# Performance work log

Measured on AMD Instinct MI355X. Metric: run time of the kernel, lower is better.

## Reference

```python
import jax, jax.numpy as jnp
import numpy as np

B, N, D = 32, 2048, 320

def _init(key, shape, fan_in):
    return jax.random.normal(key, shape, dtype=jnp.float32) / np.sqrt(fan_in).astype(np.float32)

def setup_inputs() -> dict:
    key = jax.random.key(0)
    ks = jax.random.split(key, 11)
    return {
        "x": jax.random.normal(ks[0], (B, N, D), dtype=jnp.float32),
        # downs MLP: 320->160->80
        "W1": _init(ks[1], (320, 160), 320), "b1": jnp.zeros((160,), jnp.float32),
        "W2": _init(ks[2], (160, 80), 160),  "b2": jnp.zeros((80,), jnp.float32),
        # GraphConv1d layers: 80->40, 40->5
        "Wg1": _init(ks[3], (80, 40), 80),   "bg1": jnp.zeros((40,), jnp.float32),
        "Wg2": _init(ks[4], (40, 5), 40),    "bg2": jnp.zeros((5,), jnp.float32),
        # final classifier: 5->2
        "Wf": _init(ks[5], (5, 2), 5),       "bf": jnp.zeros((2,), jnp.float32),
    }

def _euclidean_adj(h):
    # h: [B, N, C] -> row-softmax of negative squared pairwise Euclidean distance [B, N, N]
    sq = jnp.sum(h * h, axis=-1, keepdims=True)               # [B, N, 1]
    d2 = sq - 2.0 * jnp.einsum('bnc,bmc->bnm', h, h) + jnp.swapaxes(sq, -1, -2)
    return jax.nn.softmax(-d2, axis=-1)

def _graph_conv(h, W, b):
    a = _euclidean_adj(h)                                     # dynamic adjacency
    agg = jnp.einsum('bnm,bmc->bnc', a, h)                    # neighbor aggregation
    return jax.nn.relu(agg @ W + b)

def reference(x, W1, b1, W2, b2, Wg1, bg1, Wg2, bg2, Wf, bf):
    h = jax.nn.relu(x @ W1 + b1)          # [B, N, 160]
    h = jax.nn.relu(h @ W2 + b2)          # [B, N, 80]
    h = _graph_conv(h, Wg1, bg1)          # [B, N, 40]
    h = _graph_conv(h, Wg2, bg2)          # [B, N, 5]
    h = jnp.mean(h, axis=1)               # Mean() over nodes -> [B, 5]
    logits = h @ Wf + bf                  # [B, 2]
    return jax.nn.softmax(logits, axis=-1)
```

## Files before the change

kernel.cpp:

```cpp
#include <hip/hip_runtime.h>
#include <math.h>

#define BB 32
#define NN 2048
#define D_IN 320
#define H1 160
#define H2 80
#define H4 5

typedef __attribute__((ext_vector_type(8))) short short8;
typedef __attribute__((ext_vector_type(4))) short short4v;
typedef __attribute__((ext_vector_type(4))) float f32x4;
typedef __attribute__((ext_vector_type(16))) float f32x16;

__device__ inline ushort f2bf(float f) {
    union { float f; unsigned u; } v; v.f = f;
    unsigned r = v.u + 0x7fff + ((v.u >> 16) & 1);
    return (ushort)(r >> 16);
}
__device__ inline float bf2f(ushort u) {
    union { float f; unsigned u; } v; v.u = ((unsigned)u) << 16;
    return v.f;
}
__device__ inline unsigned pkbf(float hi, float lo) {
    union { float f; unsigned u; } a, b; a.f = hi; b.f = lo;
    return __builtin_amdgcn_perm(a.u + 0x8000u, b.u + 0x8000u, 0x07060302u);
}
__device__ inline float fexp2(float x) {
    float r;
    asm("v_exp_f32 %0, %1" : "=v"(r) : "v"(x));
    return r;
}
union U2S { unsigned u[2]; short4v s; };
union U4S { unsigned u[4]; short8 s; short4v h[2]; };

#define LOG2E  1.44269504088896340736f
#define TWOL2E 2.88539008177792681472f

__global__ __launch_bounds__(256) void prep_weights_kernel(
    const float* __restrict__ W1, const float* __restrict__ W2,
    const float* __restrict__ Wg1, const float* __restrict__ bg1,
    const float* __restrict__ Wg2, const float* __restrict__ bg2,
    ushort* __restrict__ Wt1, ushort* __restrict__ Wt2,
    ushort* __restrict__ Wg1B, float* __restrict__ bg1P,
    ushort* __restrict__ Wg2A, float* __restrict__ bg2P)
{
    const int id0 = blockIdx.x * 256 + threadIdx.x;
    const int stride = gridDim.x * 256;
    for (int i = id0; i < H1 * D_IN; i += stride) {
        const int j = i / D_IN, c = i % D_IN;
        Wt1[i] = f2bf(W1[c * H1 + j]);
    }
    for (int i = id0; i < H2 * H1; i += stride) {
        const int j = i / H1, c = i % H1;
        Wt2[i] = f2bf(W2[c * H2 + j]);
    }
    for (int i = id0; i < 48 * 96; i += stride) {
        const int j = i / 96, c = i % 96;
        Wg1B[i] = (j < 40 && c < 80) ? f2bf(Wg1[c * 40 + j]) : (ushort)0;
    }
    for (int i = id0; i < 32 * 48; i += stride) {
        const int j = i / 48, c = i % 48;
        const int c4 = c & 15;
        const int pos = (c & ~15) + (c4 & 3) + (((c4 >> 3) & 1) << 2) + (((c4 >> 2) & 1) << 3);
        Wg2A[j * 48 + pos] = (j < 5 && c < 40) ? f2bf(Wg2[c * 5 + j]) : (ushort)0;
    }
    if (id0 < 64) bg1P[id0] = (id0 < 40) ? bg1[id0] : 0.f;
    if (id0 < 32) bg2P[id0] = (id0 < 5) ? bg2[id0] : 0.f;
}

__global__ __launch_bounds__(256) void mlp_mfma_kernel(
    const float* __restrict__ x,
    const ushort* __restrict__ Wt1, const float* __restrict__ b1,
    const ushort* __restrict__ Wt2, const float* __restrict__ b2,
    const ushort* __restrict__ Wg1B,
    ushort* __restrict__ h2, ushort* __restrict__ V1T, float* __restrict__ sq2)
{
    constexpr int XST  = 72;
    constexpr int W1ST = 72;
    constexpr int H1ST = 168;
    constexpr int RST  = 104;

    __shared__ __attribute__((aligned(16))) ushort h1t[64 * H1ST];
    __shared__ __attribute__((aligned(16))) ushort ws1[H1 * W1ST];
    __shared__ float b1s[H1];
    __shared__ float b2s[H2];

    ushort* xs = h1t;

    const int t = threadIdx.x;
    const int lane = t & 63, w = t >> 6;
    const int colid = lane & 15, quad = lane >> 4;
    const int i = blockIdx.x;
    const int b = ((i & 7) << 2) + ((i >> 3) & 3);
    const int n0 = (i >> 5) * 64;
    const int row0 = b * NN + n0;

    if (t < H1) b1s[t] = b1[t];
    if (t < H2) b2s[t] = b2[t];

    f32x4 c1[10];
    #pragma unroll
    for (int ns = 0; ns < 10; ++ns) c1[ns] = (f32x4){0.f, 0.f, 0.f, 0.f};

    float4 xr[4];
    short8 wr[5];
    {
        #pragma unroll
        for (int i2 = 0; i2 < 4; ++i2) {
            const int id = t + i2 * 256, row = id >> 4, c4 = id & 15;
            xr[i2] = *(const float4*)&x[(size_t)(row0 + row) * D_IN + c4 * 4];
        }
        #pragma unroll
        for (int i2 = 0; i2 < 5; ++i2) {
            const int id = t + i2 * 256, j = id >> 3, part = id & 7;
            wr[i2] = *(const short8*)&Wt1[j * D_IN + part * 8];
        }
    }

    for (int kc = 0; kc < 5; ++kc) {
        if (kc) __syncthreads();
        #pragma unroll
        for (int i2 = 0; i2 < 4; ++i2) {
            const int id = t + i2 * 256, row = id >> 4, c4 = id & 15;
            uint2 up;
            up.x = pkbf(xr[i2].y, xr[i2].x);
            up.y = pkbf(xr[i2].w, xr[i2].z);
            *(uint2*)&xs[row * XST + c4 * 4] = up;
        }
        #pragma unroll
        for (int i2 = 0; i2 < 5; ++i2) {
            const int id = t + i2 * 256, j = id >> 3, part = id & 7;
            *(short8*)&ws1[j * W1ST + part * 8] = wr[i2];
        }
        __syncthreads();
        if (kc < 4) {
            const int k0 = (kc + 1) * 64;
            #pragma unroll
            for (int i2 = 0; i2 < 4; ++i2) {
                const int id = t + i2 * 256, row = id >> 4, c4 = id & 15;
                xr[i2] = *(const float4*)&x[(size_t)(row0 + row) * D_IN + k0 + c4 * 4];
            }
            #pragma unroll
            for (int i2 = 0; i2 < 5; ++i2) {
                const int id = t + i2 * 256, j = id >> 3, part = id & 7;
                wr[i2] = *(const short8*)&Wt1[j * D_IN + k0 + part * 8];
            }
        }

        short8 af[2];
        #pragma unroll
        for (int kf = 0; kf < 2; ++kf)
            af[kf] = *(const short8*)&xs[(w * 16 + colid) * XST + kf * 32 + quad * 8];
        #pragma unroll
        for (int ns = 0; ns < 10; ++ns) {
            #pragma unroll
            for (int kf = 0; kf < 2; ++kf) {
                const short8 bf = *(const short8*)&ws1[(ns * 16 + colid) * W1ST + kf * 32 + quad * 8];
                c1[ns] = __builtin_amdgcn_mfma_f32_16x16x32_bf16(af[kf], bf, c1[ns], 0, 0, 0);
            }
        }
    }
    __syncthreads();

    #pragma unroll
    for (int ns = 0; ns < 10; ++ns) {
        const float bj = b1s[ns * 16 + colid];
        #pragma unroll
        for (int r = 0; r < 4; ++r)
            h1t[(w * 16 + quad * 4 + r) * H1ST + ns * 16 + colid] =
                f2bf(fmaxf(c1[ns][r] + bj, 0.f));
    }
    __asm__ volatile("s_waitcnt lgkmcnt(0)" ::: "memory");

    short8 a2[5];
    #pragma unroll
    for (int kf = 0; kf < 5; ++kf)
        a2[kf] = *(const short8*)&h1t[(w * 16 + colid) * H1ST + kf * 32 + quad * 8];

    f32x4 c2[5];
    #pragma unroll
    for (int js = 0; js < 5; ++js) {
        f32x4 acc = (f32x4){0.f, 0.f, 0.f, 0.f};
        #pragma unroll
        for (int kf = 0; kf < 5; ++kf) {
            const short8 wb = *(const short8*)&Wt2[(js * 16 + colid) * H1 + kf * 32 + quad * 8];
            acc = __builtin_amdgcn_mfma_f32_16x16x32_bf16(a2[kf], wb, acc, 0, 0, 0);
        }
        c2[js] = acc;
    }
    __syncthreads();

    ushort* h2row = h1t;
    float rsq[4] = {0.f, 0.f, 0.f, 0.f};
    #pragma unroll
    for (int js = 0; js < 5; ++js) {
        const float bj = b2s[js * 16 + colid];
        #pragma unroll
        for (int r = 0; r < 4; ++r) {
            const ushort u = f2bf(fmaxf(c2[js][r] + bj, 0.f));
            const float vv = bf2f(u);
            rsq[r] += vv * vv;
            h2[(size_t)(row0 + w * 16 + quad * 4 + r) * 80 + js * 16 + colid] = u;
            h2row[(w * 16 + quad * 4 + r) * RST + js * 16 + colid] = u;
        }
    }
    {
        const int zr = t >> 2, zc = t & 3;
        *(short4v*)&h2row[zr * RST + 80 + zc * 4] = (short4v){0, 0, 0, 0};
    }
    __asm__ volatile("s_waitcnt lgkmcnt(0)" ::: "memory");

    short8 a3[3];
    #pragma unroll
    for (int kf = 0; kf < 3; ++kf)
        a3[kf] = *(const short8*)&h2row[(w * 16 + colid) * RST + kf * 32 + quad * 8];

    f32x4 c3[3];
    #pragma unroll
    for (int js = 0; js < 3; ++js) {
        f32x4 acc = (f32x4){0.f, 0.f, 0.f, 0.f};
        #pragma unroll
        for (int kf = 0; kf < 3; ++kf) {
            const short8 wb = *(const short8*)&Wg1B[(js * 16 + colid) * 96 + kf * 32 + quad * 8];
            acc = __builtin_amdgcn_mfma_f32_16x16x32_bf16(a3[kf], wb, acc, 0, 0, 0);
        }
        c3[js] = acc;
    }

    #pragma unroll
    for (int m = 1; m <= 8; m <<= 1)
        #pragma unroll
        for (int r = 0; r < 4; ++r) rsq[r] += __shfl_xor(rsq[r], m);
    if (colid == 0) {
        #pragma unroll
        for (int r = 0; r < 4; ++r)
            sq2[(size_t)row0 + w * 16 + quad * 4 + r] = rsq[r] * 0.5f;
    }

    ushort* Tbuf = ws1;
    #pragma unroll
    for (int js = 0; js < 3; ++js)
        #pragma unroll
        for (int r = 0; r < 4; ++r)
            Tbuf[(js * 16 + colid) * 72 + w * 16 + quad * 4 + r] = f2bf(c3[js][r]);
    __syncthreads();
    const short8 ones8 = {16256, 16256, 16256, 16256, 16256, 16256, 16256, 16256};
    for (int id = t; id < 48 * 8; id += 256) {
        const int row = id >> 3, part = id & 7;
        const short8 val = (row == 40) ? ones8 : *(const short8*)&Tbuf[row * 72 + part * 8];
        *(short8*)&V1T[((size_t)b * 48 + row) * NN + n0 + part * 8] = val;
    }
}

template<int CK, int CV, int CVS, int ONES_CH, bool HAS_OUT, bool DO_MEAN, int C_OUT>
__global__ __launch_bounds__(256, 2) void attn_conv_kernel(
    const ushort* __restrict__ h, const ushort* __restrict__ hT,
    const float* __restrict__ sqg,
    const ushort* __restrict__ WtP, const float* __restrict__ biasP,
    ushort* __restrict__ ho, ushort* __restrict__ hoT, float* __restrict__ sqo,
    float* __restrict__ mean_out)
{
    constexpr int CF   = CK / 16;
    constexpr int CSV  = CV / 32;
    constexpr int KST  = CK + 8;
    constexpr int VST  = 64 + 8;
    constexpr int KPR  = CK / 8;
    constexpr int KTOT = 64 * KPR;
    constexpr int NK   = (KTOT + 255) / 256;
    constexpr int VTOT = CVS * 8;
    constexpr int NV   = (VTOT + 255) / 256;
    constexpr int TST  = 136;
    constexpr int CS1  = ONES_CH / 32;
    constexpr int R1   = ((ONES_CH % 32) / 8) * 4 + (ONES_CH & 3);
    constexpr int BUFN = 64 * KST + CVS * VST;
    constexpr int NIT  = NN / 64;
    constexpr int NRND = NIT / 2;

    __shared__ __attribute__((aligned(16))) ushort ldsbuf[4][BUFN];
    __shared__ __attribute__((aligned(16))) float sqs[4][64];

    const int t = threadIdx.x;
    const int lane = t & 63, w = t >> 6;
    const int m32 = lane & 31, hl = lane >> 5;
    const int i = blockIdx.x;
    const int b = ((i & 7) << 2) + ((i >> 3) & 3);
    const int n0blk = (i >> 5) * 128;
    const int qrow = n0blk + w * 32 + m32;

    short8 qf[CF];
    {
        const ushort* qr = h + ((size_t)b * NN + qrow) * CK;
        #pragma unroll
        for (int c = 0; c < CF; ++c)
            qf[c] = *(const short8*)&qr[c * 16 + hl * 8];
    }
    const float nsqn = -sqg[(size_t)b * NN + qrow];

    f32x16 o[CSV];
    #pragma unroll
    for (int cs = 0; cs < CSV; ++cs)
        #pragma unroll
        for (int r = 0; r < 16; ++r) o[cs][r] = 0.f;

    short8 kregA[NK], vregA[NV]; float sqregA = 0.f;
    short8 kregB[NK], vregB[NV]; float sqregB = 0.f;

    auto loadTile = [&](int n1, short8 (&kreg)[NK], short8 (&vreg)[NV], float& sqreg) {
        const ushort* hsrc = h + ((size_t)b * NN + n1) * CK;
        #pragma unroll
        for (int i2 = 0; i2 < NK; ++i2) {
            const int id = t + i2 * 256;
            if (KTOT % 256 == 0 || id < KTOT)
                kreg[i2] = *(const short8*)&hsrc[id * 8];
        }
        #pragma unroll
        for (int i2 = 0; i2 < NV; ++i2) {
            const int id = t + i2 * 256;
            if (VTOT % 256 == 0 || id < VTOT) {
                const int c = id >> 3, pt = id & 7;
                vreg[i2] = *(const short8*)&hT[((size_t)b * CVS + c) * NN + n1 + pt * 8];
            }
        }
        if (t < 64) sqreg = sqg[(size_t)b * NN + n1 + t];
    };
    auto stageTile = [&](int buf, const short8 (&kreg)[NK], const short8 (&vreg)[NV], float sqreg) {
        ushort* Kd = ldsbuf[buf];
        ushort* Vd = ldsbuf[buf] + 64 * KST;
        #pragma unroll
        for (int i2 = 0; i2 < NK; ++i2) {
            const int id = t + i2 * 256;
            if (KTOT % 256 == 0 || id < KTOT) {
                const int row = id / KPR, pt = id % KPR;
                *(short8*)&Kd[row * KST + pt * 8] = kreg[i2];
            }
        }
        #pragma unroll
        for (int i2 = 0; i2 < NV; ++i2) {
            const int id = t + i2 * 256;
            if (VTOT % 256 == 0 || id < VTOT) {
                const int c = id >> 3, pt = id & 7;
                const int colb = ((pt >> 1) << 4) + ((pt & 1) << 2);
                U4S vv; vv.s = vreg[i2];
                *(short4v*)&Vd[c * VST + colb]     = vv.h[0];
                *(short4v*)&Vd[c * VST + colb + 8] = vv.h[1];
            }
        }
        if (t < 64) sqs[buf][t] = sqreg;
    };

    auto preloadK = [&](const ushort* Krow, short8 (&kf)[2][CF]) {
        #pragma unroll
        for (int T = 0; T < 2; ++T)
            #pragma unroll
            for (int c = 0; c < CF; ++c)
                kf[T][c] = *(const short8*)&Krow[(T * 32 + m32) * KST + c * 16 + hl * 8];
    };
    auto initST = [&](int buf, f32x16& s0, f32x16& s1) {
        #pragma unroll
        for (int g = 0; g < 4; ++g) {
            const f32x4 sm0 = *(const f32x4*)&sqs[buf][g * 8 + hl * 4];
            const f32x4 sm1 = *(const f32x4*)&sqs[buf][32 + g * 8 + hl * 4];
            #pragma unroll
            for (int r2 = 0; r2 < 4; ++r2) {
                s0[g * 4 + r2] = nsqn - sm0[r2];
                s1[g * 4 + r2] = nsqn - sm1[r2];
            }
        }
    };
    auto smfma = [&](short8 (&kf)[2][CF], f32x16& s0, f32x16& s1) {
        #pragma unroll
        for (int c = 0; c < CF; ++c) {
            s0 = __builtin_amdgcn_mfma_f32_32x32x16_bf16(kf[0][c], qf[c], s0, 0, 0, 0);
            s1 = __builtin_amdgcn_mfma_f32_32x32x16_bf16(kf[1][c], qf[c], s1, 0, 0, 0);
        }
    };
    auto readV = [&](const ushort* Vcol, short8 (&vf)[2][2][CSV]) {
        const short8 z8 = {0, 0, 0, 0, 0, 0, 0, 0};
        #pragma unroll
        for (int T = 0; T < 2; ++T)
            #pragma unroll
            for (int c = 0; c < 2; ++c)
                #pragma unroll
                for (int cs = 0; cs < CSV; ++cs) {
                    const int row = cs * 32 + m32;
                    vf[T][c][cs] = (row < CVS)
                        ? *(const short8*)&Vcol[row * VST + (T * 2 + c) * 16 + hl * 8]
                        : z8;
                }
    };
    auto expPV = [&](const f32x16& s0, const f32x16& s1, const short8 (&vf)[2][2][CSV]) {
        #pragma unroll
        for (int T = 0; T < 2; ++T) {
            const f32x16& st = T ? s1 : s0;
            float p[16];
            #pragma unroll
            for (int g = 0; g < 4; ++g)
                #pragma unroll
                for (int r2 = 0; r2 < 4; ++r2)
                    p[g * 4 + r2] = fexp2(st[g * 4 + r2] * TWOL2E);
            #pragma unroll
            for (int c = 0; c < 2; ++c) {
                U4S pk_;
                #pragma unroll
                for (int bq = 0; bq < 4; ++bq)
                    pk_.u[bq] = pkbf(p[c * 8 + bq * 2 + 1], p[c * 8 + bq * 2]);
                #pragma unroll
                for (int cs = 0; cs < CSV; ++cs)
                    o[cs] = __builtin_amdgcn_mfma_f32_32x32x16_bf16(vf[T][c][cs], pk_.s, o[cs], 0, 0, 0);
            }
        }
    };

    loadTile(0, kregA, vregA, sqregA);
    loadTile(64, kregB, vregB, sqregB);
    stageTile(0, kregA, vregA, sqregA);
    stageTile(1, kregB, vregB, sqregB);
    __syncthreads();
    loadTile(128, kregA, vregA, sqregA);
    loadTile(192, kregB, vregB, sqregB);

    #pragma unroll 1
    for (int k = 0; k < NRND; ++k) {
        const int p = k & 1;
        const ushort* K0 = ldsbuf[2 * p];
        const ushort* K1 = ldsbuf[2 * p + 1];

        f32x16 s00, s01, s10, s11;
        short8 kf[2][CF];
        preloadK(K0, kf);
        initST(2 * p, s00, s01);
        initST(2 * p + 1, s10, s11);

        if (k < NRND - 1) {
            stageTile(2 * (1 - p), kregA, vregA, sqregA);
            stageTile(2 * (1 - p) + 1, kregB, vregB, sqregB);
        }
        if (k < NRND - 2) {
            loadTile((2 * k + 4) * 64, kregA, vregA, sqregA);
            loadTile((2 * k + 5) * 64, kregB, vregB, sqregB);
        }

        smfma(kf, s00, s01);
        preloadK(K1, kf);
        smfma(kf, s10, s11);

        short8 vf[2][2][CSV];
        readV(K0 + 64 * KST, vf);
        expPV(s00, s01, vf);
        readV(K1 + 64 * KST, vf);
        expPV(s10, s11, vf);

        if (k < NRND - 1) __syncthreads();
    }

    float rsv = (hl == 0) ? o[CS1][R1] : 0.f;
    rsv += __shfl_xor(rsv, 32);
    const float rinv = 1.f / rsv;

    if constexpr (DO_MEAN) {
        float msum[4];
        #pragma unroll
        for (int r2 = 0; r2 < 4; ++r2)
            msum[r2] = fmaxf(o[0][r2] * rinv + biasP[hl * 4 + r2], 0.f);
        #pragma unroll
        for (int s = 1; s <= 16; s <<= 1)
            #pragma unroll
            for (int r2 = 0; r2 < 4; ++r2) msum[r2] += __shfl_xor(msum[r2], s);
        if (m32 == 0) {
            if (hl == 0) {
                #pragma unroll
                for (int r2 = 0; r2 < 4; ++r2)
                    atomicAdd(&mean_out[b * C_OUT + r2], msum[r2] * (1.f / NN));
            } else {
                atomicAdd(&mean_out[b * C_OUT + 4], msum[0] * (1.f / NN));
            }
        }
    }

    if constexpr (HAS_OUT) {
        float vv[CSV][16];
        float rsq = 0.f;
        #pragma unroll
        for (int cs = 0; cs < CSV; ++cs) {
            #pragma unroll
            for (int g = 0; g < 4; ++g) {
                const int jb = cs * 32 + g * 8 + hl * 4;
                const f32x4 bv = *(const f32x4*)&biasP[jb];
                float v[4];
                #pragma unroll
                for (int r2 = 0; r2 < 4; ++r2) {
                    float val = fmaxf(o[cs][g * 4 + r2] * rinv + bv[r2], 0.f);
                    if (cs == CS1 && g * 4 + r2 == R1) val = 0.f;
                    v[r2] = val;
                    vv[cs][g * 4 + r2] = val;
                }
                if (jb < 48) {
                    U2S uo;
                    uo.u[0] = pkbf(v[1], v[0]);
                    uo.u[1] = pkbf(v[3], v[2]);
                    *(short4v*)&ho[((size_t)b * NN + qrow) * 48 + jb] = uo.s;
                    #pragma unroll
                    for (int r2 = 0; r2 < 4; ++r2) {
                        const float vs = bf2f((ushort)(uo.u[r2 >> 1] >> ((r2 & 1) * 16)));
                        rsq += vs * vs;
                    }
                }
            }
        }
        const float rsq2 = rsq + __shfl_xor(rsq, 32);
        if (hl == 0) sqo[(size_t)b * NN + qrow] = rsq2 * 0.5f;

        short8 ob2[3];
        #pragma unroll
        for (int cc = 0; cc < 3; ++cc) {
            const int cs = cc >> 1, c2 = cc & 1;
            U4S ob_;
            #pragma unroll
            for (int bq = 0; bq < 4; ++bq)
                ob_.u[bq] = pkbf(vv[cs][c2 * 8 + bq * 2 + 1], vv[cs][c2 * 8 + bq * 2]);
            ob2[cc] = ob_.s;
        }
        f32x16 acc;
        #pragma unroll
        for (int r = 0; r < 16; ++r) acc[r] = 0.f;
        #pragma unroll
        for (int cc = 0; cc < 3; ++cc) {
            const short8 wa = *(const short8*)&WtP[(size_t)m32 * 48 + cc * 16 + hl * 8];
            acc = __builtin_amdgcn_mfma_f32_32x32x16_bf16(wa, ob2[cc], acc, 0, 0, 0);
        }

        ushort* Tbuf = (ushort*)ldsbuf;
        #pragma unroll
        for (int g = 0; g < 2; ++g)
            #pragma unroll
            for (int r2 = 0; r2 < 4; ++r2)
                Tbuf[(g * 8 + hl * 4 + r2) * TST + w * 32 + m32] = f2bf(acc[g * 4 + r2]);
        __syncthreads();
        const short8 ones8 = {16256, 16256, 16256, 16256, 16256, 16256, 16256, 16256};
        {
            const int row = t >> 4, part = t & 15;
            const short8 val = (row == 8) ? ones8
                             : *(const short8*)&Tbuf[row * TST + part * 8];
            *(short8*)&hoT[((size_t)b * 16 + row) * NN + n0blk + part * 8] = val;
        }
    }
}

__global__ __launch_bounds__(64) void final_kernel(
    const float* __restrict__ mean, const float* __restrict__ Wf,
    const float* __restrict__ bf, float* __restrict__ out)
{
    const int t = threadIdx.x;
    const int b = t >> 1, k = t & 1;
    float acc = bf[k];
    #pragma unroll
    for (int c = 0; c < H4; ++c) acc += mean[b * H4 + c] * Wf[c * 2 + k];
    const float other = __shfl_xor(acc, 1);
    const float mx = fmaxf(acc, other);
    const float e  = __expf(acc - mx);
    const float eo = __expf(other - mx);
    out[t] = e / (e + eo);
}

extern "C" void kernel_launch(void* const* d_in, const int* in_sizes, int n_in,
                              void* d_out, int out_size, void* d_ws, size_t ws_size,
                              hipStream_t stream) {
    const float* x   = (const float*)d_in[0];
    const float* W1  = (const float*)d_in[1];
    const float* b1  = (const float*)d_in[2];
    const float* W2  = (const float*)d_in[3];
    const float* b2  = (const float*)d_in[4];
    const float* Wg1 = (const float*)d_in[5];
    const float* bg1 = (const float*)d_in[6];
    const float* Wg2 = (const float*)d_in[7];
    const float* bg2 = (const float*)d_in[8];
    const float* Wf  = (const float*)d_in[9];
    const float* bf  = (const float*)d_in[10];

    ushort* h2   = (ushort*)d_ws;
    ushort* V1T  = h2  + (size_t)BB * NN * 80;
    float*  sq2  = (float*)(V1T + (size_t)BB * 48 * NN);
    ushort* h3   = (ushort*)(sq2 + (size_t)BB * NN);
    ushort* V2T  = h3  + (size_t)BB * NN * 48;
    float*  sq3  = (float*)(V2T + (size_t)BB * 16 * NN);
    float*  meanb = sq3 + (size_t)BB * NN;
    ushort* Wt1  = (ushort*)(meanb + 160);
    ushort* Wt2  = Wt1 + (size_t)H1 * D_IN;
    ushort* Wg1B = Wt2 + (size_t)H2 * H1;
    float*  bg1P = (float*)(Wg1B + 48 * 96);
    ushort* Wg2A = (ushort*)(bg1P + 64);
    float*  bg2P = (float*)(Wg2A + 32 * 48);

    hipMemsetAsync(meanb, 0, BB * H4 * sizeof(float), stream);

    prep_weights_kernel<<<64, 256, 0, stream>>>(W1, W2, Wg1, bg1, Wg2, bg2,
                                                Wt1, Wt2, Wg1B, bg1P, Wg2A, bg2P);
    mlp_mfma_kernel<<<BB * NN / 64, 256, 0, stream>>>(x, Wt1, b1, Wt2, b2, Wg1B,
                                                      h2, V1T, sq2);
    attn_conv_kernel<80, 64, 48, 40, true,  false, 0><<<BB * NN / 128, 256, 0, stream>>>(
        h2, V1T, sq2, Wg2A, bg1P, h3, V2T, sq3, nullptr);
    attn_conv_kernel<48, 32, 16, 8,  false, true,  5><<<BB * NN / 128, 256, 0, stream>>>(
        h3, V2T, sq3, nullptr, bg2P, nullptr, nullptr, nullptr, meanb);
    final_kernel<<<1, 64, 0, stream>>>(meanb, Wf, bf, (float*)d_out);
}
```

Measured before the change: 265.1 us.

## Software-pipeline QK and PV stages across tiles, raise MFMA priority

Measured after the change: 291.2 us. 1.1x slower.

```diff
diff --git a/kernel.cpp b/kernel.cpp
--- a/kernel.cpp
+++ b/kernel.cpp
@@ -369,11 +369,13 @@
         }
     };
     auto smfma = [&](short8 (&kf)[2][CF], f32x16& s0, f32x16& s1) {
+        __builtin_amdgcn_s_setprio(1);
         #pragma unroll
         for (int c = 0; c < CF; ++c) {
             s0 = __builtin_amdgcn_mfma_f32_32x32x16_bf16(kf[0][c], qf[c], s0, 0, 0, 0);
             s1 = __builtin_amdgcn_mfma_f32_32x32x16_bf16(kf[1][c], qf[c], s1, 0, 0, 0);
         }
+        __builtin_amdgcn_s_setprio(0);
     };
     auto readV = [&](const ushort* Vcol, short8 (&vf)[2][2][CSV]) {
         const short8 z8 = {0, 0, 0, 0, 0, 0, 0, 0};
@@ -420,39 +422,63 @@
     loadTile(128, kregA, vregA, sqregA);
     loadTile(192, kregB, vregB, sqregB);
 
+    f32x16 sC0, sC1;
+    short8 vfC[2][2][CSV];
+
+    {
+        short8 kf[2][CF];
+        f32x16 sA0, sA1;
+        preloadK(ldsbuf[0], kf);
+        initST(0, sA0, sA1);
+        smfma(kf, sA0, sA1);
+        stageTile(2, kregA, vregA, sqregA);
+        stageTile(3, kregB, vregB, sqregB);
+        preloadK(ldsbuf[1], kf);
+        initST(1, sC0, sC1);
+        smfma(kf, sC0, sC1);
+        short8 vfA[2][2][CSV];
+        readV(ldsbuf[0] + 64 * KST, vfA);
+        expPV(sA0, sA1, vfA);
+        loadTile(256, kregA, vregA, sqregA);
+        loadTile(320, kregB, vregB, sqregB);
+        readV(ldsbuf[1] + 64 * KST, vfC);
+        __syncthreads();
+    }
+
     #pragma unroll 1
-    for (int k = 0; k < NRND; ++k) {
+    for (int k = 1; k < NRND; ++k) {
         const int p = k & 1;
-        const ushort* K0 = ldsbuf[2 * p];
-        const ushort* K1 = ldsbuf[2 * p + 1];
-
-        f32x16 s00, s01, s10, s11;
+        const ushort* Kb0 = ldsbuf[2 * p];
+        const ushort* Kb1 = ldsbuf[2 * p + 1];
+
         short8 kf[2][CF];
-        preloadK(K0, kf);
-        initST(2 * p, s00, s01);
-        initST(2 * p + 1, s10, s11);
+        f32x16 sA0, sA1;
+        preloadK(Kb0, kf);
+        initST(2 * p, sA0, sA1);
+        smfma(kf, sA0, sA1);
+        expPV(sC0, sC1, vfC);
 
         if (k < NRND - 1) {
             stageTile(2 * (1 - p), kregA, vregA, sqregA);
             stageTile(2 * (1 - p) + 1, kregB, vregB, sqregB);
         }
+
+        preloadK(Kb1, kf);
+        initST(2 * p + 1, sC0, sC1);
+        smfma(kf, sC0, sC1);
+        short8 vfA[2][2][CSV];
+        readV(Kb0 + 64 * KST, vfA);
+        expPV(sA0, sA1, vfA);
+
         if (k < NRND - 2) {
             loadTile((2 * k + 4) * 64, kregA, vregA, sqregA);
             loadTile((2 * k + 5) * 64, kregB, vregB, sqregB);
         }
-
-        smfma(kf, s00, s01);
-        preloadK(K1, kf);
-        smfma(kf, s10, s11);
-
-        short8 vf[2][2][CSV];
-        readV(K0 + 64 * KST, vf);
-        expPV(s00, s01, vf);
-        readV(K1 + 64 * KST, vf);
-        expPV(s10, s11, vf);
+        readV(Kb1 + 64 * KST, vfC);
 
         if (k < NRND - 1) __syncthreads();
     }
+    expPV(sC0, sC1, vfC);
 
     float rsv = (hl == 0) ? o[CS1][R1] : 0.f;
     rsv += __shfl_xor(rsv, 32);
```
